# Optimization experiments

Measured on AMD Instinct MI355X. Metric: run time of the kernel, lower is better.

## Reference

```python
import jax, jax.numpy as jnp
import numpy as np

DT = 0.1
N_STEPS = 20
STEP_SIZE = DT / N_STEPS


def setup_inputs() -> dict:
    key = jax.random.key(0)
    ks = jax.random.split(key, 8)
    sizes = [1024, 2048, 2048, 10]
    batch = 4096
    inp = {
        "x": jax.random.uniform(ks[0], (batch, sizes[0]), dtype=jnp.float32),
        "w0": jax.random.normal(ks[1], (sizes[0], sizes[1]), dtype=jnp.float32) / np.sqrt(sizes[0]),
        "w1": jax.random.normal(ks[2], (sizes[1], sizes[2]), dtype=jnp.float32) / np.sqrt(sizes[1]),
        "w2": jax.random.normal(ks[3], (sizes[2], sizes[3]), dtype=jnp.float32) / np.sqrt(sizes[2]),
        "b0": jnp.zeros((sizes[1],), jnp.float32),
        "b1": jnp.zeros((sizes[2],), jnp.float32),
        "b2": jnp.zeros((sizes[3],), jnp.float32),
        "s1": jax.random.uniform(ks[4], (batch, sizes[1]), dtype=jnp.float32),
        "s2": jax.random.uniform(ks[5], (batch, sizes[2]), dtype=jnp.float32),
        "s3": jax.random.uniform(ks[6], (batch, sizes[3]), dtype=jnp.float32),
    }
    return inp


def reference(x, w0, w1, w2, b0, b1, b2, s1, s2, s3):
    weights = [w0, w1, w2]
    biases = [b0, b1, b2]
    sig = jax.nn.sigmoid

    def dsig(v):
        s = sig(v)
        return s * (1.0 - s)

    def body(states, _):
        st = list(states)  # [s0(=x, clamped), s1, s2, s3]
        # hidden layers (indices 1..len-2), sequential in-place semantics
        for i in range(1, 3):
            pre = sig(st[i - 1]) @ weights[i - 1] + sig(st[i + 1]) @ weights[i].T + biases[i - 1]
            grad = dsig(st[i]) * pre - st[i]
            st[i] = st[i] - STEP_SIZE * grad
        # output layer (no target / beta=0 in eval mode)
        grad = dsig(st[3]) * (sig(st[2]) @ weights[2] + biases[2]) - st[3]
        st[3] = st[3] - STEP_SIZE * grad
        return tuple(st), None

    init = (x, s1, s2, s3)
    final, _ = jax.lax.scan(body, init, None, length=N_STEPS)
    return final[-1]
```

## Files before the change

### kernel.cpp

```cpp
#include <hip/hip_runtime.h>
#include <cstdint>
#include <cstddef>

using u16 = unsigned short;
using u32 = unsigned int;

typedef __bf16 bf16x8 __attribute__((ext_vector_type(8)));
typedef float f32x4 __attribute__((ext_vector_type(4)));
typedef u16 u16x4 __attribute__((ext_vector_type(4)));

#define DEV __device__ __forceinline__

constexpr float SS = 0.1f / 20.0f;

DEV float sigm(float x) { return 1.0f / (1.0f + __expf(-x)); }

DEV u16 f2bf(float f) {
  union { float f; u32 u; } v; v.f = f;
  u32 r = v.u + 0x7FFFu + ((v.u >> 16) & 1u);
  return (u16)(r >> 16);
}
DEV float bf2f(u16 h) {
  union { u32 u; float f; } v; v.u = ((u32)h) << 16;
  return v.f;
}

__global__ void k_prep(const float* __restrict__ in, float* __restrict__ fcopy,
                       float* __restrict__ sigf32, u16* __restrict__ sigb,
                       u16* __restrict__ rawb, int n) {
  int stride = gridDim.x * blockDim.x;
  for (int i = blockIdx.x * blockDim.x + threadIdx.x; i < n; i += stride) {
    float v = in[i];
    if (fcopy) fcopy[i] = v;
    if (rawb) rawb[i] = f2bf(v);
    if (sigf32 || sigb) {
      float s = sigm(v);
      if (sigf32) sigf32[i] = s;
      if (sigb) sigb[i] = f2bf(s);
    }
  }
}

__global__ void k_transpose_bf16(const float* __restrict__ in, u16* __restrict__ out,
                                 int K, int N) {
  __shared__ float tile[32][33];
  int kb = blockIdx.x * 32, nb = blockIdx.y * 32;
  int tx = threadIdx.x & 31, ty = threadIdx.x >> 5;
#pragma unroll
  for (int i = 0; i < 4; ++i)
    tile[ty + 8 * i][tx] = in[(size_t)(kb + ty + 8 * i) * N + nb + tx];
  __syncthreads();
#pragma unroll
  for (int i = 0; i < 4; ++i)
    out[(size_t)(nb + ty + 8 * i) * K + kb + tx] = f2bf(tile[tx][ty + 8 * i]);
}

template <int MODE>
__global__ void k_gemm(const u16* __restrict__ A, const u16* __restrict__ Bt,
                       int M, int N, int K,
                       const u16* __restrict__ addcb, const float* __restrict__ bias,
                       const float* __restrict__ sig3, const float* __restrict__ w2,
                       float* __restrict__ statef, u16* __restrict__ sigb) {
  constexpr int BM = 128, BN = 128, BK = 64;
  __shared__ __align__(16) u16 Als[BM * BK];
  __shared__ __align__(16) u16 Bls[BN * BK];
  int b = blockIdx.x;
  int xcd = b & 7, slot = b >> 3;
  int tm = ((((xcd >> 1) << 3) | (slot >> 3))) * BM;
  int tn = ((((xcd & 1) << 3) | (slot & 7))) * BN;
  int tid = threadIdx.x;
  int lane = tid & 63, wid = tid >> 6;
  int l15 = lane & 15, lhi = lane >> 4;
  int wm = (wid >> 1) * 64, wn = (wid & 1) * 64;

  f32x4 acc[4][4] = {};

  const u16* Ag = A + (size_t)tm * K;
  const u16* Bg = Bt + (size_t)tn * K;

  for (int k0 = 0; k0 < K; k0 += BK) {
#pragma unroll
    for (int rd = 0; rd < 4; ++rd) {
      int S = rd * 256 + tid;
      int row = S >> 3;
      int cs = ((S & 7) ^ (row & 7)) * 8;
      __builtin_amdgcn_global_load_lds(
          (const __attribute__((address_space(1))) u32*)(Ag + (size_t)row * K + k0 + cs),
          (__attribute__((address_space(3))) u32*)(Als + S * 8), 16, 0, 0);
      __builtin_amdgcn_global_load_lds(
          (const __attribute__((address_space(1))) u32*)(Bg + (size_t)row * K + k0 + cs),
          (__attribute__((address_space(3))) u32*)(Bls + S * 8), 16, 0, 0);
    }
    __syncthreads();
#pragma unroll
    for (int s = 0; s < 2; ++s) {
      bf16x8 af[4], bfr[4];
#pragma unroll
      for (int i = 0; i < 4; ++i) {
        int row = wm + i * 16 + l15;
        af[i] = *(const bf16x8*)(Als + row * BK + (((s * 4 + lhi) ^ (row & 7)) * 8));
      }
#pragma unroll
      for (int j = 0; j < 4; ++j) {
        int row = wn + j * 16 + l15;
        bfr[j] = *(const bf16x8*)(Bls + row * BK + (((s * 4 + lhi) ^ (row & 7)) * 8));
      }
#pragma unroll
      for (int i = 0; i < 4; ++i)
#pragma unroll
        for (int j = 0; j < 4; ++j)
          acc[i][j] = __builtin_amdgcn_mfma_f32_16x16x32_bf16(bfr[j], af[i], acc[i][j], 0, 0, 0);
    }
    __syncthreads();
  }

  if constexpr (MODE == 0) {
#pragma unroll
    for (int i = 0; i < 4; ++i) {
      int gr = tm + wm + i * 16 + l15;
#pragma unroll
      for (int j = 0; j < 4; ++j) {
        int gc0 = tn + wn + j * 16 + 4 * lhi;
        u16x4 sb;
#pragma unroll
        for (int rr = 0; rr < 4; ++rr) sb[rr] = f2bf(acc[i][j][rr] + bias[gc0 + rr]);
        *(u16x4*)(sigb + (size_t)gr * N + gc0) = sb;
      }
    }
  } else if constexpr (MODE == 1) {
#pragma unroll
    for (int i = 0; i < 4; ++i) {
      int gr = tm + wm + i * 16 + l15;
#pragma unroll
      for (int j = 0; j < 4; ++j) {
        int gc0 = tn + wn + j * 16 + 4 * lhi;
        size_t idx = (size_t)gr * N + gc0;
        u16x4 ab = *(const u16x4*)(addcb + idx);
        f32x4 old = *(const f32x4*)(statef + idx);
        f32x4 nv; u16x4 sb;
#pragma unroll
        for (int rr = 0; rr < 4; ++rr) {
          float pre = acc[i][j][rr] + bf2f(ab[rr]);
          float o = old[rr];
          float sg = sigm(o);
          float n = o - SS * (sg * (1.0f - sg) * pre - o);
          nv[rr] = n; sb[rr] = f2bf(sigm(n));
        }
        *(f32x4*)(statef + idx) = nv;
        *(u16x4*)(sigb + idx) = sb;
      }
    }
  } else {
    float s3v[4][10];
#pragma unroll
    for (int i = 0; i < 4; ++i) {
      int gr = tm + wm + i * 16 + l15;
#pragma unroll
      for (int k = 0; k < 10; ++k) s3v[i][k] = sig3[gr * 10 + k];
    }
#pragma unroll
    for (int j = 0; j < 4; ++j) {
      int gc0 = tn + wn + j * 16 + 4 * lhi;
      float wv[4][10]; f32x4 bb;
#pragma unroll
      for (int rr = 0; rr < 4; ++rr) {
        bb[rr] = bias[gc0 + rr];
#pragma unroll
        for (int k = 0; k < 10; ++k) wv[rr][k] = w2[(gc0 + rr) * 10 + k];
      }
#pragma unroll
      for (int i = 0; i < 4; ++i) {
        int gr = tm + wm + i * 16 + l15;
        size_t idx = (size_t)gr * N + gc0;
        f32x4 old = *(const f32x4*)(statef + idx);
        f32x4 nv; u16x4 sb;
#pragma unroll
        for (int rr = 0; rr < 4; ++rr) {
          float ex = bb[rr];
#pragma unroll
          for (int k = 0; k < 10; ++k) ex += s3v[i][k] * wv[rr][k];
          float pre = acc[i][j][rr] + ex;
          float o = old[rr];
          float sg = sigm(o);
          float n = o - SS * (sg * (1.0f - sg) * pre - o);
          nv[rr] = n; sb[rr] = f2bf(sigm(n));
        }
        *(f32x4*)(statef + idx) = nv;
        *(u16x4*)(sigb + idx) = sb;
      }
    }
  }
}

__global__ void k_out(const u16* __restrict__ sigs2b, const float* __restrict__ w2,
                      const float* __restrict__ b2, float* __restrict__ s3f,
                      float* __restrict__ sigs3f, float* __restrict__ outOrNull) {
  int tid = threadIdx.x;
  int r = tid >> 4, l16 = tid & 15;
  int row = blockIdx.x * 16 + r;
  float acc[10] = {};
  const u16* arow = sigs2b + (size_t)row * 2048;
  for (int kb = l16; kb < 256; kb += 16) {
    u16x4 v0 = *(const u16x4*)(arow + kb * 8);
    u16x4 v1 = *(const u16x4*)(arow + kb * 8 + 4);
    float a[8];
#pragma unroll
    for (int e = 0; e < 4; ++e) { a[e] = bf2f(v0[e]); a[e + 4] = bf2f(v1[e]); }
    const float* wr = w2 + (size_t)kb * 80;
#pragma unroll
    for (int e = 0; e < 8; ++e)
#pragma unroll
      for (int n = 0; n < 10; ++n) acc[n] += a[e] * wr[e * 10 + n];
  }
#pragma unroll
  for (int m = 1; m < 16; m <<= 1)
#pragma unroll
    for (int n = 0; n < 10; ++n) acc[n] += __shfl_xor(acc[n], m, 64);
  if (l16 < 10) {
    float pre = 0.0f;
#pragma unroll
    for (int n = 0; n < 10; ++n)
      if (l16 == n) pre = acc[n];
    pre += b2[l16];
    size_t idx = (size_t)row * 10 + l16;
    float old = s3f[idx];
    float sg = sigm(old);
    float nv = old - SS * (sg * (1.0f - sg) * pre - old);
    s3f[idx] = nv;
    sigs3f[idx] = sigm(nv);
    if (outOrNull) outOrNull[idx] = nv;
  }
}

extern "C" void kernel_launch(void* const* d_in, const int* in_sizes, int n_in,
                              void* d_out, int out_size, void* d_ws, size_t ws_size,
                              hipStream_t stream) {
  const float* x  = (const float*)d_in[0];
  const float* w0 = (const float*)d_in[1];
  const float* w1 = (const float*)d_in[2];
  const float* w2 = (const float*)d_in[3];
  const float* b0 = (const float*)d_in[4];
  const float* b1 = (const float*)d_in[5];
  const float* b2 = (const float*)d_in[6];
  const float* s1 = (const float*)d_in[7];
  const float* s2 = (const float*)d_in[8];
  const float* s3 = (const float*)d_in[9];
  float* out = (float*)d_out;

  uint8_t* p = (uint8_t*)d_ws;
  auto alloc = [&](size_t bytes) {
    uint8_t* r = p;
    p += (bytes + 255) & ~(size_t)255;
    return r;
  };
  float* s1f    = (float*)alloc(4096ull * 2048 * 4);
  float* s2f    = (float*)alloc(4096ull * 2048 * 4);
  u16*   addcb  = (u16*)alloc(4096ull * 2048 * 2);
  u16*   sigs1b = (u16*)alloc(4096ull * 2048 * 2);
  u16*   sigs2b = (u16*)alloc(4096ull * 2048 * 2);
  u16*   sigxb  = (u16*)alloc(4096ull * 1024 * 2);
  u16*   w1b    = (u16*)alloc(2048ull * 2048 * 2);
  u16*   w1tb   = (u16*)alloc(2048ull * 2048 * 2);
  u16*   w0tb   = (u16*)alloc(2048ull * 1024 * 2);
  float* s3f    = (float*)alloc(4096ull * 10 * 4);
  float* sigs3f = (float*)alloc(4096ull * 10 * 4);
  (void)ws_size; (void)in_sizes; (void)n_in; (void)out_size;

  auto grid = [](int n) { int g = (n + 255) / 256; return g > 2048 ? 2048 : g; };

  k_prep<<<grid(4096 * 1024), 256, 0, stream>>>(x, nullptr, nullptr, sigxb, nullptr, 4096 * 1024);
  k_prep<<<grid(2048 * 2048), 256, 0, stream>>>(w1, nullptr, nullptr, nullptr, w1b, 2048 * 2048);
  k_prep<<<grid(4096 * 2048), 256, 0, stream>>>(s1, s1f, nullptr, nullptr, nullptr, 4096 * 2048);
  k_prep<<<grid(4096 * 2048), 256, 0, stream>>>(s2, s2f, nullptr, sigs2b, nullptr, 4096 * 2048);
  k_prep<<<grid(40960), 256, 0, stream>>>(s3, s3f, sigs3f, nullptr, nullptr, 40960);
  k_transpose_bf16<<<dim3(1024 / 32, 2048 / 32), 256, 0, stream>>>(w0, w0tb, 1024, 2048);
  k_transpose_bf16<<<dim3(2048 / 32, 2048 / 32), 256, 0, stream>>>(w1, w1tb, 2048, 2048);

  k_gemm<0><<<512, 256, 0, stream>>>(sigxb, w0tb, 4096, 2048, 1024,
                                     nullptr, b0, nullptr, nullptr, nullptr, addcb);

  for (int t = 0; t < 20; ++t) {
    k_gemm<1><<<512, 256, 0, stream>>>(sigs2b, w1b, 4096, 2048, 2048,
                                       addcb, nullptr, nullptr, nullptr, s1f, sigs1b);
    k_gemm<2><<<512, 256, 0, stream>>>(sigs1b, w1tb, 4096, 2048, 2048,
                                       nullptr, b1, sigs3f, w2, s2f, sigs2b);
    k_out<<<256, 256, 0, stream>>>(sigs2b, w2, b2, s3f, sigs3f, (t == 19) ? out : nullptr);
  }
}
```

Before: 2.910 ms.

## Double-buffer LDS tiles in GEMM to overlap global loads with MFMA

```diff
diff --git a/kernel.cpp b/kernel.cpp
--- a/kernel.cpp
+++ b/kernel.cpp
@@ -56,14 +56,15 @@
 }
 
 template <int MODE>
+__launch_bounds__(256)
 __global__ void k_gemm(const u16* __restrict__ A, const u16* __restrict__ Bt,
                        int M, int N, int K,
                        const u16* __restrict__ addcb, const float* __restrict__ bias,
                        const float* __restrict__ sig3, const float* __restrict__ w2,
                        float* __restrict__ statef, u16* __restrict__ sigb) {
   constexpr int BM = 128, BN = 128, BK = 64;
-  __shared__ __align__(16) u16 Als[BM * BK];
-  __shared__ __align__(16) u16 Bls[BN * BK];
+  __shared__ __align__(16) u16 Als[2][BM * BK];
+  __shared__ __align__(16) u16 Bls[2][BN * BK];
   int b = blockIdx.x;
   int xcd = b & 7, slot = b >> 3;
   int tm = ((((xcd >> 1) << 3) | (slot >> 3))) * BM;
@@ -73,12 +74,12 @@
   int l15 = lane & 15, lhi = lane >> 4;
   int wm = (wid >> 1) * 64, wn = (wid & 1) * 64;
 
-  f32x4 acc[4][4] = {};
-
   const u16* Ag = A + (size_t)tm * K;
   const u16* Bg = Bt + (size_t)tn * K;
 
-  for (int k0 = 0; k0 < K; k0 += BK) {
+  f32x4 acc[4][4] = {};
+
+  auto stage = [&](int buf, int k0) {
 #pragma unroll
     for (int rd = 0; rd < 4; ++rd) {
       int S = rd * 256 + tid;
@@ -86,24 +87,26 @@
       int cs = ((S & 7) ^ (row & 7)) * 8;
       __builtin_amdgcn_global_load_lds(
           (const __attribute__((address_space(1))) u32*)(Ag + (size_t)row * K + k0 + cs),
-          (__attribute__((address_space(3))) u32*)(Als + S * 8), 16, 0, 0);
+          (__attribute__((address_space(3))) u32*)(&Als[buf][0] + S * 8), 16, 0, 0);
       __builtin_amdgcn_global_load_lds(
           (const __attribute__((address_space(1))) u32*)(Bg + (size_t)row * K + k0 + cs),
-          (__attribute__((address_space(3))) u32*)(Bls + S * 8), 16, 0, 0);
-    }
-    __syncthreads();
+          (__attribute__((address_space(3))) u32*)(&Bls[buf][0] + S * 8), 16, 0, 0);
+    }
+  };
+
+  auto compute = [&](int buf) {
 #pragma unroll
     for (int s = 0; s < 2; ++s) {
       bf16x8 af[4], bfr[4];
 #pragma unroll
       for (int i = 0; i < 4; ++i) {
         int row = wm + i * 16 + l15;
-        af[i] = *(const bf16x8*)(Als + row * BK + (((s * 4 + lhi) ^ (row & 7)) * 8));
+        af[i] = *(const bf16x8*)(&Als[buf][0] + row * BK + (((s * 4 + lhi) ^ (row & 7)) * 8));
       }
 #pragma unroll
       for (int j = 0; j < 4; ++j) {
         int row = wn + j * 16 + l15;
-        bfr[j] = *(const bf16x8*)(Bls + row * BK + (((s * 4 + lhi) ^ (row & 7)) * 8));
+        bfr[j] = *(const bf16x8*)(&Bls[buf][0] + row * BK + (((s * 4 + lhi) ^ (row & 7)) * 8));
       }
 #pragma unroll
       for (int i = 0; i < 4; ++i)
@@ -111,8 +114,32 @@
         for (int j = 0; j < 4; ++j)
           acc[i][j] = __builtin_amdgcn_mfma_f32_16x16x32_bf16(bfr[j], af[i], acc[i][j], 0, 0, 0);
     }
-    __syncthreads();
-  }
+  };
+
+  const int nt = K / BK;
+  stage(0, 0);
+  asm volatile("s_waitcnt vmcnt(0)" ::: "memory");
+  __builtin_amdgcn_s_barrier();
+  asm volatile("" ::: "memory");
+  int t = 0;
+  for (; t + 2 < nt; t += 2) {
+    stage(1, (t + 1) * BK);
+    compute(0);
+    asm volatile("s_waitcnt vmcnt(0) lgkmcnt(0)" ::: "memory");
+    __builtin_amdgcn_s_barrier();
+    asm volatile("" ::: "memory");
+    stage(0, (t + 2) * BK);
+    compute(1);
+    asm volatile("s_waitcnt vmcnt(0) lgkmcnt(0)" ::: "memory");
+    __builtin_amdgcn_s_barrier();
+    asm volatile("" ::: "memory");
+  }
+  stage(1, (nt - 1) * BK);
+  compute(0);
+  asm volatile("s_waitcnt vmcnt(0) lgkmcnt(0)" ::: "memory");
+  __builtin_amdgcn_s_barrier();
+  asm volatile("" ::: "memory");
+  compute(1);
 
   if constexpr (MODE == 0) {
 #pragma unroll
```

New measurement: 2.678 ms. -7.9%, faster.
